# Kernel tuning notes

Hardware: AMD Instinct MI355X
Metric: run time of the kernel (lower is better)

Reference implementation:

```python
import jax, jax.numpy as jnp
import numpy as np

H, W = 512, 512
CHUNK = 128            # gaussians blended per scan step
BLUR = 0.3             # antialiasing dilation (as in 3DGS EWA low-pass)
ALPHA_MIN = 1.0 / 255.0
ALPHA_MAX = 0.99


def setup_inputs() -> dict:
    key = jax.random.key(0)
    k = jax.random.split(key, 6)
    N = 8192
    means2D = jax.random.uniform(k[0], (N, 2), jnp.float32) * jnp.array([W, H], jnp.float32)
    colors = jax.random.uniform(k[1], (N, 3), jnp.float32)
    opacities = jax.random.uniform(k[2], (N, 1), jnp.float32)
    scales = jax.random.uniform(k[3], (N, 2), jnp.float32) * 15.0 + 1.0   # pixels
    rotations = jax.random.uniform(k[4], (N, 1), jnp.float32) * (2.0 * np.pi)
    depths = jax.random.uniform(k[5], (N,), jnp.float32)
    background = jnp.zeros((3,), jnp.float32)
    return dict(means2D=means2D, colors=colors, opacities=opacities,
                scales=scales, rotations=rotations, depths=depths,
                background=background)


def _rasterize(means2D, colors, opacities, scales, rotations, depths, background):
    # depth sort: front (small depth) first
    order = jnp.argsort(depths)
    m = means2D[order]                 # [N,2] (x,y)
    col = colors[order]                # [N,3]
    op = opacities[order][:, 0]        # [N]
    s = scales[order]                  # [N,2]
    th = rotations[order][:, 0]        # [N]

    # 2D covariance  Sigma = R diag(s^2) R^T
    c, si = jnp.cos(th), jnp.sin(th)
    sx2, sy2 = s[:, 0] ** 2, s[:, 1] ** 2
    A = c * c * sx2 + si * si * sy2
    Cc = si * si * sx2 + c * c * sy2
    B = c * si * (sx2 - sy2)
    det = A * Cc - B * B
    # antialiasing: dilate covariance, compensate opacity
    A2, C2 = A + BLUR, Cc + BLUR
    det2 = A2 * C2 - B * B
    op = op * jnp.sqrt(jnp.maximum(det / det2, 0.0))
    invdet = 1.0 / det2
    ia, ib, ic = C2 * invdet, -B * invdet, A2 * invdet   # Sigma^-1 entries

    # pixel centers
    ys, xs = jnp.meshgrid(jnp.arange(H, dtype=jnp.float32) + 0.5,
                          jnp.arange(W, dtype=jnp.float32) + 0.5, indexing='ij')

    N = m.shape[0]
    nchunk = N // CHUNK
    chunk = lambda a: a.reshape((nchunk, CHUNK) + a.shape[1:])
    gs = (chunk(m), chunk(col), chunk(op), chunk(ia), chunk(ib), chunk(ic))

    def step(carry, g):
        T, acc = carry                       # T:[H,W] transmittance, acc:[3,H,W]
        gm, gcol, gop, gia, gib, gic = g     # per-chunk [C,...]
        dx = xs[None] - gm[:, 0, None, None]                 # [C,H,W]
        dy = ys[None] - gm[:, 1, None, None]
        power = (-0.5 * (gia[:, None, None] * dx * dx + gic[:, None, None] * dy * dy)
                 - gib[:, None, None] * dx * dy)
        alpha = jnp.minimum(ALPHA_MAX, gop[:, None, None] * jnp.exp(power))
        alpha = jnp.where(alpha < ALPHA_MIN, 0.0, alpha)     # skip tiny splats (as CUDA)
        one_m = 1.0 - alpha
        cum = jnp.cumprod(one_m, axis=0)                     # inclusive
        Twithin = jnp.concatenate([jnp.ones_like(cum[:1]), cum[:-1]], 0)  # exclusive
        w = alpha * Twithin * T[None]                        # blend weight per gaussian
        acc = acc + jnp.einsum('nc,nhw->chw', gcol, w)
        T = T * cum[-1]
        return (T, acc), None

    init = (jnp.ones((H, W), jnp.float32), jnp.zeros((3, H, W), jnp.float32))
    (T, acc), _ = jax.lax.scan(step, init, gs)
    color = acc + background[:, None, None] * T[None]        # [3,H,W]
    return color


def reference(means2D, colors, opacities, scales, rotations, depths, background):
    return _rasterize(means2D, colors, opacities, scales, rotations, depths, background)
```

## Files before the change

kernel.cpp:

```cpp
#include <hip/hip_runtime.h>
#include <stdint.h>

#define HH 512
#define WW 512
#define ALPHA_MIN_C (1.0f/255.0f)
#define ALPHA_MAX_C 0.99f
#define BLUR_C 0.3f
#define TERM_EPS 1.0e-4f

#define JCHUNK 512
__global__ __launch_bounds__(256) void rank_kernel(const float* __restrict__ depths,
                                                   int N, int* __restrict__ rank) {
    __shared__ uint32_t sk[JCHUNK];
    const int tid = threadIdx.x;
    const int ngb = N >> 8;
    const int gb = blockIdx.x % ngb;
    const int j0 = (blockIdx.x / ngb) * JCHUNK;
    for (int i = tid; i < JCHUNK; i += 256)
        sk[i] = __float_as_uint(depths[j0 + i]);
    __syncthreads();
    const int g = gb * 256 + tid;
    const uint32_t mb = __float_as_uint(depths[g]);
    const int glim = g - j0;
    int cnt = 0;
    const uint4* sk4 = (const uint4*)sk;
#pragma unroll 8
    for (int q = 0; q < JCHUNK / 4; ++q) {
        uint4 v = sk4[q];
        const int i4 = q * 4;
        cnt += (v.x < mb) || (v.x == mb && (i4 + 0) < glim);
        cnt += (v.y < mb) || (v.y == mb && (i4 + 1) < glim);
        cnt += (v.z < mb) || (v.z == mb && (i4 + 2) < glim);
        cnt += (v.w < mb) || (v.w == mb && (i4 + 3) < glim);
    }
    atomicAdd(&rank[g], cnt);
}

__global__ __launch_bounds__(256) void prep_kernel(
    const float* __restrict__ means, const float* __restrict__ colors,
    const float* __restrict__ ops, const float* __restrict__ scales,
    const float* __restrict__ rots, const int* __restrict__ rank, int N,
    float4* __restrict__ pA, float4* __restrict__ pB,
    float* __restrict__ pC, float* __restrict__ pR) {
    int g = blockIdx.x * 256 + threadIdx.x;
    if (g >= N) return;
    int pos = rank[g];
    float mx = means[2*g], my = means[2*g+1];
    float th = rots[g];
    float c = cosf(th), si = sinf(th);
    float sx = scales[2*g], sy = scales[2*g+1];
    float sx2 = sx*sx, sy2 = sy*sy;
    float A  = c*c*sx2 + si*si*sy2;
    float Cc = si*si*sx2 + c*c*sy2;
    float B  = c*si*(sx2 - sy2);
    float det = A*Cc - B*B;
    float A2 = A + BLUR_C, C2 = Cc + BLUR_C;
    float det2 = A2*C2 - B*B;
    float op = ops[g] * sqrtf(fmaxf(det/det2, 0.0f));
    float invd = 1.0f/det2;
    float ia = C2*invd, ib = -B*invd, ic = A2*invd;
    float mid = 0.5f*(A2+C2);
    float lam = mid + sqrtf(fmaxf(mid*mid - det2, 0.0f));
    float r2;
    if (op < ALPHA_MIN_C) {
        r2 = -1.0f;
    } else {
        float t = __logf(op * 255.0f);
        r2 = fmaxf(2.0f * lam * t, 0.0f) * 1.0001f + 0.25f;
    }
    pA[pos] = make_float4(mx, my, ia, ib);
    pB[pos] = make_float4(ic, op, colors[3*g], colors[3*g+1]);
    pC[pos] = colors[3*g+2];
    pR[pos] = r2;
}

__global__ __launch_bounds__(256) void blend_kernel(
    const float4* __restrict__ pA, const float4* __restrict__ pB,
    const float* __restrict__ pC, const float* __restrict__ pR,
    const float* __restrict__ bg, int N, float* __restrict__ out) {
    __shared__ float4 sA[256];
    __shared__ float4 sB[256];
    __shared__ float  sC[256];
    __shared__ float  sR[256];
    __shared__ int    wcnt[4];
    const int tid = threadIdx.x;
    const int lane = tid & 63, wid = tid >> 6;
    const int tileX = blockIdx.x & 31, tileY = blockIdx.x >> 5;
    const int qx = tileX*16 + (wid & 1)*8;
    const int qy = tileY*16 + (wid >> 1)*8;
    const int px = qx + (lane & 7);
    const int py = qy + (lane >> 3);
    const float fx = px + 0.5f, fy = py + 0.5f;
    const float qx0 = qx + 0.5f, qx1 = qx + 7.5f;
    const float qy0 = qy + 0.5f, qy1 = qy + 7.5f;
    const float x0 = tileX*16 + 0.5f, x1 = x0 + 15.0f;
    const float y0 = tileY*16 + 0.5f, y1 = y0 + 15.0f;
    float T = 1.0f, accR = 0.0f, accG = 0.0f, accB = 0.0f;

    float4 a = pA[tid];
    float4 b = pB[tid];
    float cb = pC[tid];
    float r2 = pR[tid];

    for (int base = 0; base < N; base += 256) {
        float nx = fminf(fmaxf(a.x, x0), x1) - a.x;
        float ny = fminf(fmaxf(a.y, y0), y1) - a.y;
        bool flag = (nx*nx + ny*ny) <= r2;
        uint64_t mask = __ballot(flag);
        if (lane == 0) wcnt[wid] = __popcll(mask);
        __syncthreads();
        int off = __popcll(mask & ((1ull << lane) - 1ull));
        for (int w2 = 0; w2 < wid; ++w2) off += wcnt[w2];
        const int M = wcnt[0] + wcnt[1] + wcnt[2] + wcnt[3];
        if (flag) { sA[off] = a; sB[off] = b; sC[off] = cb; sR[off] = r2; }
        __syncthreads();
        const int gn = base + 256 + tid;
        if (gn < N) { a = pA[gn]; b = pB[gn]; cb = pC[gn]; r2 = pR[gn]; }
        if (!__all(T < TERM_EPS)) {
            for (int i = 0; i < M; ++i) {
                float4 ga = sA[i];
                float wx = fminf(fmaxf(ga.x, qx0), qx1) - ga.x;
                float wy = fminf(fmaxf(ga.y, qy0), qy1) - ga.y;
                if (wx*wx + wy*wy > sR[i]) continue;
                float4 gb = sB[i];
                float dx = fx - ga.x, dy = fy - ga.y;
                float power = -0.5f*(ga.z*dx*dx + gb.x*dy*dy) - ga.w*dx*dy;
                float alpha = fminf(ALPHA_MAX_C, gb.y * __expf(power));
                if (alpha >= ALPHA_MIN_C) {
                    float w = alpha * T;
                    accR += gb.z * w;
                    accG += gb.w * w;
                    accB += sC[i] * w;
                    T *= (1.0f - alpha);
                }
            }
        }
        if (__syncthreads_and(T < TERM_EPS)) break;
    }
    const int pix = py*WW + px;
    out[pix]             = accR + bg[0]*T;
    out[pix +   HH*WW]   = accG + bg[1]*T;
    out[pix + 2*HH*WW]   = accB + bg[2]*T;
}

extern "C" void kernel_launch(void* const* d_in, const int* in_sizes, int n_in,
                              void* d_out, int out_size, void* d_ws, size_t ws_size,
                              hipStream_t stream) {
    const float* means   = (const float*)d_in[0];
    const float* colors  = (const float*)d_in[1];
    const float* ops     = (const float*)d_in[2];
    const float* scales  = (const float*)d_in[3];
    const float* rots    = (const float*)d_in[4];
    const float* depths  = (const float*)d_in[5];
    const float* bg      = (const float*)d_in[6];
    const int N = in_sizes[0] / 2;

    char* ws = (char*)d_ws;
    float4* pA  = (float4*)(ws);
    float4* pB  = (float4*)(ws + (size_t)N*16);
    float*  pC  = (float*)(ws + (size_t)N*32);
    float*  pR  = (float*)(ws + (size_t)N*36);
    int*    rank= (int*)  (ws + (size_t)N*40);

    hipMemsetAsync(rank, 0, (size_t)N*4, stream);

    const int ngb = N / 256;
    const int njb = N / JCHUNK;
    rank_kernel<<<dim3(ngb*njb), dim3(256), 0, stream>>>(depths, N, rank);
    prep_kernel<<<dim3((N+255)/256), dim3(256), 0, stream>>>(
        means, colors, ops, scales, rots, rank, N, pA, pB, pC, pR);
    blend_kernel<<<dim3((WW/16)*(HH/16)), dim3(256), 0, stream>>>(
        pA, pB, pC, pR, bg, N, (float*)d_out);
}
```

Baseline: 163.8 us.

## Double-buffer gaussian staging and broadcast records via readlane in blend loop

The blend kernel now double-buffers the per-chunk shared staging so culling of the next chunk overlaps blending of the current one, removing one barrier per chunk. Each gaussian record is read from LDS as one lane-distributed load and broadcast to all lanes with readlane, instead of several LDS broadcast reads. The per-wave 8x8 quad cull test is dropped. Prep folds the -0.5 and log2e factors into the conic so exp2f can be used with FMAs, and packs color-blue with radius into a float2. In exchange it uses more LDS and evaluates gaussians that the finer quad test used to skip.

```diff
diff --git a/kernel.cpp b/kernel.cpp
--- a/kernel.cpp
+++ b/kernel.cpp
@@ -7,6 +7,11 @@
 #define ALPHA_MAX_C 0.99f
 #define BLUR_C 0.3f
 #define TERM_EPS 1.0e-4f
+#define LOG2E 1.4426950408889634f
+
+__device__ __forceinline__ float rlf(float v, int l) {
+    return __uint_as_float((unsigned)__builtin_amdgcn_readlane(__float_as_uint(v), l));
+}
 
 #define JCHUNK 512
 __global__ __launch_bounds__(256) void rank_kernel(const float* __restrict__ depths,
@@ -40,8 +45,7 @@
     const float* __restrict__ means, const float* __restrict__ colors,
     const float* __restrict__ ops, const float* __restrict__ scales,
     const float* __restrict__ rots, const int* __restrict__ rank, int N,
-    float4* __restrict__ pA, float4* __restrict__ pB,
-    float* __restrict__ pC, float* __restrict__ pR) {
+    float4* __restrict__ pA, float4* __restrict__ pB, float2* __restrict__ pCR) {
     int g = blockIdx.x * 256 + threadIdx.x;
     if (g >= N) return;
     int pos = rank[g];
@@ -59,6 +63,7 @@
     float op = ops[g] * sqrtf(fmaxf(det/det2, 0.0f));
     float invd = 1.0f/det2;
     float ia = C2*invd, ib = -B*invd, ic = A2*invd;
+    float iaF = -0.5f*LOG2E*ia, icF = -0.5f*LOG2E*ic, ibF = -LOG2E*ib;
     float mid = 0.5f*(A2+C2);
     float lam = mid + sqrtf(fmaxf(mid*mid - det2, 0.0f));
     float r2;
@@ -68,74 +73,91 @@
         float t = __logf(op * 255.0f);
         r2 = fmaxf(2.0f * lam * t, 0.0f) * 1.0001f + 0.25f;
     }
-    pA[pos] = make_float4(mx, my, ia, ib);
-    pB[pos] = make_float4(ic, op, colors[3*g], colors[3*g+1]);
-    pC[pos] = colors[3*g+2];
-    pR[pos] = r2;
+    pA[pos]  = make_float4(mx, my, iaF, ibF);
+    pB[pos]  = make_float4(icF, op, colors[3*g], colors[3*g+1]);
+    pCR[pos] = make_float2(colors[3*g+2], r2);
 }
 
 __global__ __launch_bounds__(256) void blend_kernel(
     const float4* __restrict__ pA, const float4* __restrict__ pB,
-    const float* __restrict__ pC, const float* __restrict__ pR,
-    const float* __restrict__ bg, int N, float* __restrict__ out) {
-    __shared__ float4 sA[256];
-    __shared__ float4 sB[256];
-    __shared__ float  sC[256];
-    __shared__ float  sR[256];
-    __shared__ int    wcnt[4];
+    const float2* __restrict__ pCR, const float* __restrict__ bg,
+    int N, float* __restrict__ out) {
+    __shared__ __align__(16) float sG[2][4*64*12 + 16];
+    __shared__ int swcnt[2][4];
     const int tid = threadIdx.x;
     const int lane = tid & 63, wid = tid >> 6;
     const int tileX = blockIdx.x & 31, tileY = blockIdx.x >> 5;
-    const int qx = tileX*16 + (wid & 1)*8;
-    const int qy = tileY*16 + (wid >> 1)*8;
-    const int px = qx + (lane & 7);
-    const int py = qy + (lane >> 3);
+    const int px = tileX*16 + (tid & 15);
+    const int py = tileY*16 + (tid >> 4);
     const float fx = px + 0.5f, fy = py + 0.5f;
-    const float qx0 = qx + 0.5f, qx1 = qx + 7.5f;
-    const float qy0 = qy + 0.5f, qy1 = qy + 7.5f;
     const float x0 = tileX*16 + 0.5f, x1 = x0 + 15.0f;
     const float y0 = tileY*16 + 0.5f, y1 = y0 + 15.0f;
+    const int fld = lane & 15;
     float T = 1.0f, accR = 0.0f, accG = 0.0f, accB = 0.0f;
+    const int nch = N >> 8;
 
-    float4 a = pA[tid];
-    float4 b = pB[tid];
-    float cb = pC[tid];
-    float r2 = pR[tid];
-
-    for (int base = 0; base < N; base += 256) {
+    float4 a = pA[tid]; float4 b = pB[tid]; float2 c2 = pCR[tid];
+    {
         float nx = fminf(fmaxf(a.x, x0), x1) - a.x;
         float ny = fminf(fmaxf(a.y, y0), y1) - a.y;
-        bool flag = (nx*nx + ny*ny) <= r2;
-        uint64_t mask = __ballot(flag);
-        if (lane == 0) wcnt[wid] = __popcll(mask);
-        __syncthreads();
-        int off = __popcll(mask & ((1ull << lane) - 1ull));
-        for (int w2 = 0; w2 < wid; ++w2) off += wcnt[w2];
-        const int M = wcnt[0] + wcnt[1] + wcnt[2] + wcnt[3];
-        if (flag) { sA[off] = a; sB[off] = b; sC[off] = cb; sR[off] = r2; }
-        __syncthreads();
-        const int gn = base + 256 + tid;
-        if (gn < N) { a = pA[gn]; b = pB[gn]; cb = pC[gn]; r2 = pR[gn]; }
+        bool flag = (nx*nx + ny*ny) <= c2.y;
+        uint64_t m = __ballot(flag);
+        if (flag) {
+            int off = __popcll(m & ((1ull << lane) - 1ull));
+            float* rec = &sG[0][(wid*64 + off)*12];
+            *(float4*)rec = a; *(float4*)(rec+4) = b; rec[8] = c2.x;
+        }
+        if (lane == 0) swcnt[0][wid] = (int)__popcll(m);
+    }
+    if (256 + tid < N) { a = pA[256+tid]; b = pB[256+tid]; c2 = pCR[256+tid]; }
+    __syncthreads();
+
+    int cur = 0;
+    for (int k = 0; k < nch; ++k) {
+        const int nxt = cur ^ 1;
+        if (k + 1 < nch) {
+            float nx = fminf(fmaxf(a.x, x0), x1) - a.x;
+            float ny = fminf(fmaxf(a.y, y0), y1) - a.y;
+            bool flag = (nx*nx + ny*ny) <= c2.y;
+            uint64_t m = __ballot(flag);
+            if (flag) {
+                int off = __popcll(m & ((1ull << lane) - 1ull));
+                float* rec = &sG[nxt][(wid*64 + off)*12];
+                *(float4*)rec = a; *(float4*)(rec+4) = b; rec[8] = c2.x;
+            }
+            if (lane == 0) swcnt[nxt][wid] = (int)__popcll(m);
+            const int gn = (k + 2) * 256 + tid;
+            if (gn < N) { a = pA[gn]; b = pB[gn]; c2 = pCR[gn]; }
+        }
         if (!__all(T < TERM_EPS)) {
-            for (int i = 0; i < M; ++i) {
-                float4 ga = sA[i];
-                float wx = fminf(fmaxf(ga.x, qx0), qx1) - ga.x;
-                float wy = fminf(fmaxf(ga.y, qy0), qy1) - ga.y;
-                if (wx*wx + wy*wy > sR[i]) continue;
-                float4 gb = sB[i];
-                float dx = fx - ga.x, dy = fy - ga.y;
-                float power = -0.5f*(ga.z*dx*dx + gb.x*dy*dy) - ga.w*dx*dy;
-                float alpha = fminf(ALPHA_MAX_C, gb.y * __expf(power));
-                if (alpha >= ALPHA_MIN_C) {
-                    float w = alpha * T;
-                    accR += gb.z * w;
-                    accG += gb.w * w;
-                    accB += sC[i] * w;
-                    T *= (1.0f - alpha);
+            int cv = swcnt[cur][lane & 3];
+#pragma unroll
+            for (int w2 = 0; w2 < 4; ++w2) {
+                const int cnt = __builtin_amdgcn_readlane(cv, w2);
+                const float* seg = &sG[cur][w2*64*12];
+                float rv = seg[fld];
+                for (int i = 0; i < cnt; ++i) {
+                    float rvn = seg[(i+1)*12 + fld];
+                    float mx = rlf(rv,0), my = rlf(rv,1);
+                    float ia = rlf(rv,2), ib = rlf(rv,3), ic = rlf(rv,4);
+                    float op = rlf(rv,5);
+                    float cr = rlf(rv,6), cg = rlf(rv,7), cb2 = rlf(rv,8);
+                    float dx = fx - mx, dy = fy - my;
+                    float p = fmaf(ia, dx*dx, fmaf(ic, dy*dy, ib*(dx*dy)));
+                    float al = fminf(ALPHA_MAX_C, op * exp2f(p));
+                    if (al >= ALPHA_MIN_C) {
+                        float w = al * T;
+                        accR = fmaf(cr, w, accR);
+                        accG = fmaf(cg, w, accG);
+                        accB = fmaf(cb2, w, accB);
+                        T = fmaf(-al, T, T);
+                    }
+                    rv = rvn;
                 }
             }
         }
         if (__syncthreads_and(T < TERM_EPS)) break;
+        cur = nxt;
     }
     const int pix = py*WW + px;
     out[pix]             = accR + bg[0]*T;
@@ -158,8 +180,7 @@
     char* ws = (char*)d_ws;
     float4* pA  = (float4*)(ws);
     float4* pB  = (float4*)(ws + (size_t)N*16);
-    float*  pC  = (float*)(ws + (size_t)N*32);
-    float*  pR  = (float*)(ws + (size_t)N*36);
+    float2* pCR = (float2*)(ws + (size_t)N*32);
     int*    rank= (int*)  (ws + (size_t)N*40);
 
     hipMemsetAsync(rank, 0, (size_t)N*4, stream);
@@ -168,7 +189,7 @@
     const int njb = N / JCHUNK;
     rank_kernel<<<dim3(ngb*njb), dim3(256), 0, stream>>>(depths, N, rank);
     prep_kernel<<<dim3((N+255)/256), dim3(256), 0, stream>>>(
-        means, colors, ops, scales, rots, rank, N, pA, pB, pC, pR);
+        means, colors, ops, scales, rots, rank, N, pA, pB, pCR);
     blend_kernel<<<dim3((WW/16)*(HH/16)), dim3(256), 0, stream>>>(
-        pA, pB, pC, pR, bg, N, (float*)d_out);
+        pA, pB, pCR, bg, N, (float*)d_out);
 }
```

Measured after the change: 166.9 us. About the same (+1.9%).
